# Performance work log

Hardware: AMD Instinct MI355X
Metric: run time of the kernel (lower is better)

The kernel has to match this reference:

```python
import jax, jax.numpy as jnp
import numpy as np

B, D, S = 16384, 2048, 512      # batch, input_dim, sideinfo_dim
E, H1, H2 = 8, 1024, 512        # subexpert_num, subexpert_unit
EPS = 1e-5                       # BatchNorm eps (torch default)


def setup_inputs() -> dict:
    key = jax.random.key(0)
    ks = jax.random.split(key, 16)
    inp = {
        "input": jax.random.normal(ks[0], (B, D), jnp.float32),
        "sideinfo": jax.random.normal(ks[1], (B, S), jnp.float32),
        # expert layer 1: Linear(D->H1) per expert, batched over E
        "W1": jax.random.normal(ks[2], (E, D, H1), jnp.float32) / np.sqrt(D),
        "b1": jax.random.normal(ks[3], (E, H1), jnp.float32) * 0.01,
        "gamma1": 1.0 + 0.01 * jax.random.normal(ks[4], (E, H1), jnp.float32),
        "beta1": jax.random.normal(ks[5], (E, H1), jnp.float32) * 0.01,
        "mean1": jax.random.normal(ks[6], (E, H1), jnp.float32) * 0.01,
        "var1": jax.random.uniform(ks[7], (E, H1), jnp.float32, 0.5, 1.5),
        # expert layer 2: Linear(H1->H2) per expert
        "W2": jax.random.normal(ks[8], (E, H1, H2), jnp.float32) / np.sqrt(H1),
        "b2": jax.random.normal(ks[9], (E, H2), jnp.float32) * 0.01,
        "gamma2": 1.0 + 0.01 * jax.random.normal(ks[10], (E, H2), jnp.float32),
        "beta2": jax.random.normal(ks[11], (E, H2), jnp.float32) * 0.01,
        "mean2": jax.random.normal(ks[12], (E, H2), jnp.float32) * 0.01,
        "var2": jax.random.uniform(ks[13], (E, H2), jnp.float32, 0.5, 1.5),
        # gate: Linear(S->E) + softmax
        "Wg": jax.random.normal(ks[14], (S, E), jnp.float32) / np.sqrt(S),
        "bg": jax.random.normal(ks[15], (E,), jnp.float32) * 0.01,
    }
    return inp


def _bn(x, gamma, beta, mean, var):
    # eval-mode BatchNorm1d with per-expert running stats; x: [B,E,H]
    return (x - mean) * (gamma * jax.lax.rsqrt(var + EPS)) + beta


def reference(input, sideinfo, W1, b1, gamma1, beta1, mean1, var1,
              W2, b2, gamma2, beta2, mean2, var2, Wg, bg):
    # all E expert MLPs as two batched GEMMs (dropout is identity in eval)
    h = jnp.einsum('bd,edh->beh', input, W1) + b1            # [B,E,H1]
    h = jax.nn.relu(_bn(h, gamma1, beta1, mean1, var1))
    o = jnp.einsum('beh,eho->beo', h, W2) + b2               # [B,E,H2]
    o = jax.nn.relu(_bn(o, gamma2, beta2, mean2, var2))
    gate = jax.nn.softmax(sideinfo @ Wg + bg, axis=1)        # [B,E]
    return jnp.einsum('beo,be->bo', o, gate)                 # [B,H2]
```

## Files before the change

kernel.cpp:

```cpp
#include <hip/hip_runtime.h>
#include <hip/hip_bf16.h>

static constexpr int B_  = 16384;
static constexpr int D_  = 2048;
static constexpr int S_  = 512;
static constexpr int E_  = 8;
static constexpr int H1_ = 1024;
static constexpr int H2_ = 512;
static constexpr float EPS_ = 1e-5f;

typedef __bf16 bf16x8 __attribute__((ext_vector_type(8)));
typedef float  f32x4  __attribute__((ext_vector_type(4)));

static __device__ __forceinline__ unsigned short f2bf(float f) {
    unsigned u = __float_as_uint(f);
    unsigned r = (u + 0x7fffu + ((u >> 16) & 1u)) >> 16;
    return (unsigned short)r;
}


__global__ void cvt_bf16_kernel(const float* __restrict__ in, ushort* __restrict__ out, long n) {
    long i = ((long)blockIdx.x * blockDim.x + threadIdx.x) * 4;
    long stride = (long)gridDim.x * blockDim.x * 4;
    for (; i < n; i += stride) {
        float4 v = *(const float4*)(in + i);
        ushort4 o;
        o.x = f2bf(v.x); o.y = f2bf(v.y); o.z = f2bf(v.z); o.w = f2bf(v.w);
        *(ushort4*)(out + i) = o;
    }
}

__global__ void transpose_cvt_kernel(const float* __restrict__ in, ushort* __restrict__ out,
                                     int R, int C) {
    __shared__ float t[64][65];
    int nbr = R >> 6, nbc = C >> 6;
    int bid = blockIdx.x;
    int e = bid / (nbr * nbc);
    int rem = bid % (nbr * nbc);
    int br = (rem / nbc) << 6, bc = (rem % nbc) << 6;
    const float* ip = in + (size_t)e * R * C;
    ushort* op = out + (size_t)e * R * C;
    int tcol = (threadIdx.x & 15) * 4;
    int trow = threadIdx.x >> 4;
#pragma unroll
    for (int p = 0; p < 4; p++) {
        int r = trow + p * 16;
        float4 v = *(const float4*)(ip + (size_t)(br + r) * C + bc + tcol);
        t[r][tcol + 0] = v.x; t[r][tcol + 1] = v.y; t[r][tcol + 2] = v.z; t[r][tcol + 3] = v.w;
    }
    __syncthreads();
#pragma unroll
    for (int p = 0; p < 4; p++) {
        int c = trow + p * 16;
        ushort4 o;
        o.x = f2bf(t[tcol + 0][c]);
        o.y = f2bf(t[tcol + 1][c]);
        o.z = f2bf(t[tcol + 2][c]);
        o.w = f2bf(t[tcol + 3][c]);
        *(ushort4*)(op + (size_t)(bc + c) * R + br + tcol) = o;
    }
}

__global__ void fold_bn_kernel(const float* __restrict__ gamma, const float* __restrict__ beta,
                               const float* __restrict__ mean, const float* __restrict__ var,
                               const float* __restrict__ bias,
                               float* __restrict__ Sv, float* __restrict__ Tv, int n) {
    int i = blockIdx.x * 256 + threadIdx.x;
    if (i < n) {
        float s = gamma[i] * rsqrtf(var[i] + EPS_);
        Sv[i] = s;
        Tv[i] = (bias[i] - mean[i]) * s + beta[i];
    }
}

__global__ void gate_kernel(const float* __restrict__ side, const float* __restrict__ Wg,
                            const float* __restrict__ bg, float* __restrict__ gate) {
    int wid = threadIdx.x >> 6, lane = threadIdx.x & 63;
    int b = blockIdx.x * 4 + wid;
    const float* sp = side + (size_t)b * S_ + lane * 8;
    float4 v0 = *(const float4*)sp;
    float4 v1 = *(const float4*)(sp + 4);
    float sv[8] = {v0.x, v0.y, v0.z, v0.w, v1.x, v1.y, v1.z, v1.w};
    float acc[E_] = {0,0,0,0,0,0,0,0};
    const float* wrow = Wg + (size_t)(lane * 8) * E_;
#pragma unroll
    for (int j = 0; j < 8; j++) {
        float4 w0 = *(const float4*)(wrow + j * E_);
        float4 w1 = *(const float4*)(wrow + j * E_ + 4);
        acc[0] += sv[j] * w0.x; acc[1] += sv[j] * w0.y;
        acc[2] += sv[j] * w0.z; acc[3] += sv[j] * w0.w;
        acc[4] += sv[j] * w1.x; acc[5] += sv[j] * w1.y;
        acc[6] += sv[j] * w1.z; acc[7] += sv[j] * w1.w;
    }
#pragma unroll
    for (int off = 32; off; off >>= 1)
#pragma unroll
        for (int e = 0; e < E_; e++) acc[e] += __shfl_xor(acc[e], off, 64);
    float m = -1e30f;
#pragma unroll
    for (int e = 0; e < E_; e++) { acc[e] += bg[e]; m = fmaxf(m, acc[e]); }
    float s = 0.f;
#pragma unroll
    for (int e = 0; e < E_; e++) { acc[e] = __expf(acc[e] - m); s += acc[e]; }
    float inv = 1.f / s;
    if (lane < E_) gate[(size_t)b * E_ + lane] = acc[lane] * inv;
}


__device__ __forceinline__ void g2lds16(const void* g, void* l) {
    __builtin_amdgcn_global_load_lds((const __attribute__((address_space(1))) unsigned int*)g,
                                     (__attribute__((address_space(3))) unsigned int*)l,
                                     16, 0, 0);
}

#define BAR()      asm volatile("s_barrier" ::: "memory")
#define WAITVM(n)  asm volatile("s_waitcnt vmcnt(" #n ")" ::: "memory")
#define MFMA(a,b,c) __builtin_amdgcn_mfma_f32_16x16x32_bf16((a),(b),(c),0,0,0)


template<int EPI>
__global__ __launch_bounds__(512, 2)
void gemm8(const ushort* __restrict__ A, const ushort* __restrict__ Bt, long aBatch,
           const float* __restrict__ Sv, const float* __restrict__ Tv,
           ushort* __restrict__ hout, float* __restrict__ outp, const float* __restrict__ gate,
           int M, int N, int K, int tilesN, int tilesM)
{
    extern __shared__ char smem[];

    const int NT  = K >> 6;
    const int tpe = tilesM * tilesN;

    const int nwg = gridDim.x, per = nwg >> 3;
    const int b0  = blockIdx.x;
    const int bid = (b0 & 7) * per + (b0 >> 3);

    const int e   = bid / tpe;
    const int rem = bid % tpe;
    const int tm  = rem / tilesN, tn = rem % tilesN;

    const char* aBase = (const char*)(A + (size_t)e * aBatch + (size_t)tm * 256 * K);
    const char* bBase = (const char*)(Bt + (size_t)e * N * K + (size_t)tn * 256 * K);
    const size_t rowB = (size_t)K * 2;
    const size_t half2 = 64 * rowB;
    const size_t half1 = 128 * rowB;

    const int tid = threadIdx.x, w = tid >> 6, lane = tid & 63;
    const int wm = w >> 2, wn = w & 3;

    const int srow = tid >> 3;
    const int scol_sw = ((tid & 7) * 16) ^ ((srow & 7) << 4);
    const int ldsW = w * 1024;

    const int lr = lane & 15;
    const int cks0 = ((lane >> 4) * 16) ^ ((lane & 7) << 4);
    const int cks1 = (64 + (lane >> 4) * 16) ^ ((lane & 7) << 4);
    const char* rdA0 = smem + 65536 + (wm * 128 + lr) * 128 + cks0;
    const char* rdA1 = smem + 65536 + (wm * 128 + lr) * 128 + cks1;
    const char* rdB0 = smem + (wn * 64 + lr) * 128 + cks0;
    const char* rdB1 = smem + (wn * 64 + lr) * 128 + cks1;

#define STG(gp, ldsoff) do { \
        g2lds16((gp), smem + (ldsoff)); \
        g2lds16((gp) + half2, smem + (ldsoff) + 8192); } while (0)

    const char* ga = aBase + (size_t)srow * rowB + scol_sw;
    const char* gb = bBase + (size_t)srow * rowB + scol_sw;

    f32x4 acc[8][4] = {};
    bf16x8 aC[4], aN[4], bC[4], bN[4];

    STG(ga,         65536 + 0 + 0     + ldsW);
    STG(ga + half1, 65536 + 0 + 16384 + ldsW);
    STG(gb,         0     + 0 + 0     + ldsW);
    STG(gb + half1, 0     + 0 + 16384 + ldsW);
    WAITVM(0);
    BAR();

#pragma unroll
    for (int mf = 0; mf < 4; ++mf) aC[mf] = *(const bf16x8*)(rdA0 + mf * 2048);
#pragma unroll
    for (int nf = 0; nf < 4; ++nf) bC[nf] = *(const bf16x8*)(rdB0 + nf * 2048);

    const char* spA0 = ga + 128;
    const char* spA1 = ga + half1 + 128;
    const char* spB0 = gb + 128;
    const char* spB1 = gb + half1 + 128;

#pragma unroll 2
    for (int t = 0; t < NT; ++t) {
        const int bi   = t & 1;
        const int oR   = bi * 32768;
        const int oRN  = (bi ^ 1) * 32768;
        const int oSA  = 65536 + (bi ^ 1) * 32768;
        const int oSB  = (bi ^ 1) * 32768;
        const bool more = (t < NT - 1);

#pragma unroll
        for (int mf = 0; mf < 4; ++mf) aN[mf] = *(const bf16x8*)(rdA0 + oR + (4 + mf) * 2048);
        if (more) {
            STG(spA0, oSA + 0 + ldsW);
            STG(spA1, oSA + 16384 + ldsW);
        }
        __builtin_amdgcn_s_setprio(1);
#pragma unroll
        for (int mf = 0; mf < 4; ++mf)
#pragma unroll
            for (int nf = 0; nf < 4; ++nf)
                acc[mf][nf] = MFMA(aC[mf], bC[nf], acc[mf][nf]);
        __builtin_amdgcn_s_setprio(0);

#pragma unroll
        for (int mf = 0; mf < 4; ++mf) aC[mf] = *(const bf16x8*)(rdA1 + oR + mf * 2048);
#pragma unroll
        for (int nf = 0; nf < 4; ++nf) bN[nf] = *(const bf16x8*)(rdB1 + oR + nf * 2048);
        if (more) STG(spB0, oSB + 0 + ldsW);
        __builtin_amdgcn_s_setprio(1);
#pragma unroll
        for (int mf = 0; mf < 4; ++mf)
#pragma unroll
            for (int nf = 0; nf < 4; ++nf)
                acc[4 + mf][nf] = MFMA(aN[mf], bC[nf], acc[4 + mf][nf]);
        __builtin_amdgcn_s_setprio(0);

#pragma unroll
        for (int mf = 0; mf < 4; ++mf) aN[mf] = *(const bf16x8*)(rdA1 + oR + (4 + mf) * 2048);
        if (more) STG(spB1, oSB + 16384 + ldsW);
        __builtin_amdgcn_s_setprio(1);
#pragma unroll
        for (int mf = 0; mf < 4; ++mf)
#pragma unroll
            for (int nf = 0; nf < 4; ++nf)
                acc[mf][nf] = MFMA(aC[mf], bN[nf], acc[mf][nf]);
        __builtin_amdgcn_s_setprio(0);

        __builtin_amdgcn_s_setprio(1);
#pragma unroll
        for (int mf = 0; mf < 4; ++mf)
#pragma unroll
            for (int nf = 0; nf < 4; ++nf)
                acc[4 + mf][nf] = MFMA(aN[mf], bN[nf], acc[4 + mf][nf]);
        __builtin_amdgcn_s_setprio(0);

        if (more) {
            WAITVM(0);
            BAR();
#pragma unroll
            for (int mf = 0; mf < 4; ++mf) aC[mf] = *(const bf16x8*)(rdA0 + oRN + mf * 2048);
#pragma unroll
            for (int nf = 0; nf < 4; ++nf) bC[nf] = *(const bf16x8*)(rdB0 + oRN + nf * 2048);
        }

        spA0 += 128; spA1 += 128; spB0 += 128; spB1 += 128;
    }

    const int rbase = tm * 256 + wm * 128 + (lane >> 4) * 4;
    const int cbase = tn * 256 + wn * 64 + lr;
    if (EPI == 1) {
#pragma unroll
        for (int nf = 0; nf < 4; ++nf) {
            const int col = cbase + nf * 16;
            const float s = Sv[e * N + col];
            const float tt = Tv[e * N + col];
#pragma unroll
            for (int mf = 0; mf < 8; ++mf) {
                const int row0 = rbase + mf * 16;
                f32x4 v = acc[mf][nf];
#pragma unroll
                for (int r = 0; r < 4; ++r) {
                    float x = v[r] * s + tt;
                    x = x > 0.f ? x : 0.f;
                    hout[((size_t)e * M + row0 + r) * N + col] = f2bf(x);
                }
            }
        }
    }
#undef STG
}


__global__ __launch_bounds__(512, 2)
void gemm2e(const ushort* __restrict__ H, const ushort* __restrict__ W2T,
            const float* __restrict__ Sv, const float* __restrict__ Tv,
            const float* __restrict__ gate, float* __restrict__ outp)
{
    extern __shared__ char smem[];

    const int b0 = blockIdx.x;
    const int bid = (b0 & 7) * 32 + (b0 >> 3);
    const int tm = bid >> 1, tn = bid & 1;

    const size_t rowB  = (size_t)H1_ * 2;
    const size_t strAE = (size_t)B_ * H1_ * 2;
    const size_t strBE = (size_t)H2_ * H1_ * 2;
    const size_t half2 = 64 * rowB;
    const size_t halfB = 128 * rowB;

    const int tid = threadIdx.x, w = tid >> 6, lane = tid & 63;
    const int wm = w >> 2, wn = w & 3;

    const int srow = tid >> 3;
    const int scol_sw = ((tid & 7) * 16) ^ ((srow & 7) << 4);
    const int ldsW = w * 1024;

    const int lr = lane & 15;
    const int cks0 = ((lane >> 4) * 16) ^ ((lane & 7) << 4);
    const int cks1 = (64 + (lane >> 4) * 16) ^ ((lane & 7) << 4);
    const char* rdA0 = smem + (wm * 64 + lr) * 128 + cks0;
    const char* rdA1 = smem + (wm * 64 + lr) * 128 + cks1;
    const char* rdB0 = smem + (wn * 64 + lr) * 128 + cks0;
    const char* rdB1 = smem + (wn * 64 + lr) * 128 + cks1;

    const char* ga = (const char*)H + (size_t)tm * 128 * rowB + (size_t)srow * rowB + scol_sw;
    const char* gb = (const char*)W2T + (size_t)tn * 256 * rowB + (size_t)srow * rowB + scol_sw;

#define STG6(gAp, gBp, aOff, bOff) do { \
        g2lds16((gAp),                 smem + (aOff) + 0     + ldsW); \
        g2lds16((gAp) + half2,         smem + (aOff) + 8192  + ldsW); \
        g2lds16((gBp),                 smem + (bOff) + 0     + ldsW); \
        g2lds16((gBp) + half2,         smem + (bOff) + 8192  + ldsW); \
        g2lds16((gBp) + halfB,         smem + (bOff) + 16384 + ldsW); \
        g2lds16((gBp) + halfB + half2, smem + (bOff) + 24576 + ldsW); } while (0)

    f32x4 acc[4][4] = {};
    f32x4 oacc[4][4] = {};
    bf16x8 a0[4], a1[4], b0v[4], b1v[4];

    int aCur = 98304, aN1 = 114688, aN2 = 131072;
    int bCur = 0,     bN1 = 32768,  bN2 = 65536;

    STG6(ga, gb, aCur, bCur);
    STG6(ga + 128, gb + 128, aN1, bN1);
    WAITVM(6);
    BAR();

#pragma unroll
    for (int mf = 0; mf < 4; ++mf) a0[mf] = *(const bf16x8*)(rdA0 + aCur + mf * 2048);
#pragma unroll
    for (int nf = 0; nf < 4; ++nf) b0v[nf] = *(const bf16x8*)(rdB0 + bCur + nf * 2048);

    const int rbase = tm * 128 + wm * 64 + (lane >> 4) * 4;
    const int cbase = tn * 256 + wn * 64 + lr;

    for (int t = 0; t < 128; ++t) {
        const int t2 = t + 2;
        const bool moreS = (t2 < 128);
        const bool moreT = (t < 127);

        const char* gA2 = ga + (size_t)(t2 >> 4) * strAE + (t2 & 15) * 128;
        const char* gB2 = gb + (size_t)(t2 >> 4) * strBE + (t2 & 15) * 128;

#pragma unroll
        for (int mf = 0; mf < 4; ++mf) a1[mf] = *(const bf16x8*)(rdA1 + aCur + mf * 2048);
#pragma unroll
        for (int nf = 0; nf < 4; ++nf) b1v[nf] = *(const bf16x8*)(rdB1 + bCur + nf * 2048);
        if (moreS) STG6(gA2, gB2, aN2, bN2);
        __builtin_amdgcn_s_setprio(1);
#pragma unroll
        for (int mf = 0; mf < 4; ++mf)
#pragma unroll
            for (int nf = 0; nf < 4; ++nf)
                acc[mf][nf] = MFMA(a0[mf], b0v[nf], acc[mf][nf]);
        __builtin_amdgcn_s_setprio(0);

        __builtin_amdgcn_s_setprio(1);
#pragma unroll
        for (int mf = 0; mf < 4; ++mf)
#pragma unroll
            for (int nf = 0; nf < 4; ++nf)
                acc[mf][nf] = MFMA(a1[mf], b1v[nf], acc[mf][nf]);
        __builtin_amdgcn_s_setprio(0);

        if (moreT) {
            if (moreS) { WAITVM(6); } else { WAITVM(0); }
            BAR();
#pragma unroll
            for (int mf = 0; mf < 4; ++mf) a0[mf] = *(const bf16x8*)(rdA0 + aN1 + mf * 2048);
#pragma unroll
            for (int nf = 0; nf < 4; ++nf) b0v[nf] = *(const bf16x8*)(rdB0 + bN1 + nf * 2048);
        }

        if ((t & 15) == 15) {
            const int e = t >> 4;
            float sc[4], tc[4];
#pragma unroll
            for (int nf = 0; nf < 4; ++nf) {
                sc[nf] = Sv[e * H2_ + cbase + nf * 16];
                tc[nf] = Tv[e * H2_ + cbase + nf * 16];
            }
#pragma unroll
            for (int mf = 0; mf < 4; ++mf) {
#pragma unroll
                for (int r = 0; r < 4; ++r) {
                    const int row = rbase + mf * 16 + r;
                    const float g = gate[(size_t)row * E_ + e];
#pragma unroll
                    for (int nf = 0; nf < 4; ++nf) {
                        float x = acc[mf][nf][r] * sc[nf] + tc[nf];
                        x = x > 0.f ? x : 0.f;
                        oacc[mf][nf][r] += g * x;
                    }
                }
            }
#pragma unroll
            for (int mf = 0; mf < 4; ++mf)
#pragma unroll
                for (int nf = 0; nf < 4; ++nf)
                    acc[mf][nf] = (f32x4){0.f, 0.f, 0.f, 0.f};
        }

        const int ta = aCur; aCur = aN1; aN1 = aN2; aN2 = ta;
        const int tb = bCur; bCur = bN1; bN1 = bN2; bN2 = tb;
    }

#pragma unroll
    for (int mf = 0; mf < 4; ++mf) {
#pragma unroll
        for (int r = 0; r < 4; ++r) {
            const int row = rbase + mf * 16 + r;
#pragma unroll
            for (int nf = 0; nf < 4; ++nf)
                outp[(size_t)row * H2_ + cbase + nf * 16] = oacc[mf][nf][r];
        }
    }
#undef STG6
}


extern "C" void kernel_launch(void* const* d_in, const int* in_sizes, int n_in,
                              void* d_out, int out_size, void* d_ws, size_t ws_size,
                              hipStream_t stream) {
    (void)in_sizes; (void)n_in; (void)out_size; (void)ws_size;

    const float* input    = (const float*)d_in[0];
    const float* sideinfo = (const float*)d_in[1];
    const float* W1   = (const float*)d_in[2];
    const float* b1   = (const float*)d_in[3];
    const float* g1   = (const float*)d_in[4];
    const float* be1  = (const float*)d_in[5];
    const float* m1   = (const float*)d_in[6];
    const float* v1   = (const float*)d_in[7];
    const float* W2   = (const float*)d_in[8];
    const float* b2   = (const float*)d_in[9];
    const float* g2   = (const float*)d_in[10];
    const float* be2  = (const float*)d_in[11];
    const float* m2   = (const float*)d_in[12];
    const float* v2   = (const float*)d_in[13];
    const float* Wg   = (const float*)d_in[14];
    const float* bg   = (const float*)d_in[15];

    char* w = (char*)d_ws;
    size_t off = 0;
    auto carve = [&](size_t bytes) {
        void* p = w + off;
        off += (bytes + 255) & ~(size_t)255;
        return p;
    };
    ushort* Abf  = (ushort*)carve((size_t)B_ * D_ * 2);
    ushort* W1T  = (ushort*)carve((size_t)E_ * H1_ * D_ * 2);
    ushort* W2T  = (ushort*)carve((size_t)E_ * H2_ * H1_ * 2);
    ushort* hbuf = (ushort*)carve((size_t)E_ * B_ * H1_ * 2);
    float*  S1   = (float*)carve((size_t)E_ * H1_ * 4);
    float*  T1   = (float*)carve((size_t)E_ * H1_ * 4);
    float*  S2   = (float*)carve((size_t)E_ * H2_ * 4);
    float*  T2   = (float*)carve((size_t)E_ * H2_ * 4);
    float*  gatep = (float*)carve((size_t)B_ * E_ * 4);

    float* outp = (float*)d_out;

    hipFuncSetAttribute(reinterpret_cast<const void*>(&gemm8<1>),
                        hipFuncAttributeMaxDynamicSharedMemorySize, 131072);
    hipFuncSetAttribute(reinterpret_cast<const void*>(&gemm2e),
                        hipFuncAttributeMaxDynamicSharedMemorySize, 147456);

    cvt_bf16_kernel<<<4096, 256, 0, stream>>>(input, Abf, (long)B_ * D_);
    transpose_cvt_kernel<<<E_ * (D_ / 64) * (H1_ / 64), 256, 0, stream>>>(W1, W1T, D_, H1_);
    transpose_cvt_kernel<<<E_ * (H1_ / 64) * (H2_ / 64), 256, 0, stream>>>(W2, W2T, H1_, H2_);
    fold_bn_kernel<<<(E_ * H1_ + 255) / 256, 256, 0, stream>>>(g1, be1, m1, v1, b1, S1, T1, E_ * H1_);
    fold_bn_kernel<<<(E_ * H2_ + 255) / 256, 256, 0, stream>>>(g2, be2, m2, v2, b2, S2, T2, E_ * H2_);
    gate_kernel<<<B_ / 4, 256, 0, stream>>>(sideinfo, Wg, bg, gatep);

    gemm8<1><<<E_ * (B_ / 256) * (H1_ / 256), 512, 131072, stream>>>(
        Abf, W1T, 0L, S1, T1, hbuf, nullptr, nullptr, B_, H1_, D_, H1_ / 256, B_ / 256);

    gemm2e<<<(B_ / 128) * (H2_ / 256), 512, 147456, stream>>>(
        hbuf, W2T, S2, T2, gatep, outp);
}
```

Before: 742.8 us.

## Triple-buffer B tiles in LDS to prefetch two K-steps ahead

Adds a third LDS buffer for the weight (B) operand in the first expert GEMM so its global-to-LDS copies are issued two iterations ahead, while A remains double-buffered. The wait before each barrier now allows the most recent B copy to stay in flight. This is meant to hide more global load latency behind MFMA work. In exchange, dynamic LDS grows to 160KB and buffer rotation logic adds register and control overhead.

Measured after the change: 705.2 us, median of 2. 1.05x faster.

```diff
diff --git a/kernel.cpp b/kernel.cpp
--- a/kernel.cpp
+++ b/kernel.cpp
@@ -154,8 +154,8 @@
     const int lr = lane & 15;
     const int cks0 = ((lane >> 4) * 16) ^ ((lane & 7) << 4);
     const int cks1 = (64 + (lane >> 4) * 16) ^ ((lane & 7) << 4);
-    const char* rdA0 = smem + 65536 + (wm * 128 + lr) * 128 + cks0;
-    const char* rdA1 = smem + 65536 + (wm * 128 + lr) * 128 + cks1;
+    const char* rdA0 = smem + 98304 + (wm * 128 + lr) * 128 + cks0;
+    const char* rdA1 = smem + 98304 + (wm * 128 + lr) * 128 + cks1;
     const char* rdB0 = smem + (wn * 64 + lr) * 128 + cks0;
     const char* rdB1 = smem + (wn * 64 + lr) * 128 + cks1;
 
@@ -169,11 +169,15 @@
     f32x4 acc[8][4] = {};
     bf16x8 aC[4], aN[4], bC[4], bN[4];
 
-    STG(ga,         65536 + 0 + 0     + ldsW);
-    STG(ga + half1, 65536 + 0 + 16384 + ldsW);
-    STG(gb,         0     + 0 + 0     + ldsW);
-    STG(gb + half1, 0     + 0 + 16384 + ldsW);
-    WAITVM(0);
+    int bCur = 0, bN1 = 32768, bN2 = 65536;
+
+    STG(ga,                98304 + 0 + 0     + ldsW);
+    STG(ga + half1,        98304 + 0 + 16384 + ldsW);
+    STG(gb,                0     + 0     + ldsW);
+    STG(gb + half1,        0     + 16384 + ldsW);
+    STG(gb + 128,          32768 + 0     + ldsW);
+    STG(gb + half1 + 128,  32768 + 16384 + ldsW);
+    WAITVM(4);
     BAR();
 
 #pragma unroll
@@ -183,21 +187,21 @@
 
     const char* spA0 = ga + 128;
     const char* spA1 = ga + half1 + 128;
-    const char* spB0 = gb + 128;
-    const char* spB1 = gb + half1 + 128;
+    const char* spB0 = gb + 256;
+    const char* spB1 = gb + half1 + 256;
 
 #pragma unroll 2
     for (int t = 0; t < NT; ++t) {
-        const int bi   = t & 1;
-        const int oR   = bi * 32768;
-        const int oRN  = (bi ^ 1) * 32768;
-        const int oSA  = 65536 + (bi ^ 1) * 32768;
-        const int oSB  = (bi ^ 1) * 32768;
-        const bool more = (t < NT - 1);
-
-#pragma unroll
-        for (int mf = 0; mf < 4; ++mf) aN[mf] = *(const bf16x8*)(rdA0 + oR + (4 + mf) * 2048);
-        if (more) {
+        const int bi    = t & 1;
+        const int oRA   = bi * 32768;
+        const int oRAN  = (bi ^ 1) * 32768;
+        const int oSA   = 98304 + (bi ^ 1) * 32768;
+        const bool moreA = (t < NT - 1);
+        const bool moreB = (t < NT - 2);
+
+#pragma unroll
+        for (int mf = 0; mf < 4; ++mf) aN[mf] = *(const bf16x8*)(rdA0 + oRA + (4 + mf) * 2048);
+        if (moreA) {
             STG(spA0, oSA + 0 + ldsW);
             STG(spA1, oSA + 16384 + ldsW);
         }
@@ -210,10 +214,10 @@
         __builtin_amdgcn_s_setprio(0);
 
 #pragma unroll
-        for (int mf = 0; mf < 4; ++mf) aC[mf] = *(const bf16x8*)(rdA1 + oR + mf * 2048);
-#pragma unroll
-        for (int nf = 0; nf < 4; ++nf) bN[nf] = *(const bf16x8*)(rdB1 + oR + nf * 2048);
-        if (more) STG(spB0, oSB + 0 + ldsW);
+        for (int mf = 0; mf < 4; ++mf) aC[mf] = *(const bf16x8*)(rdA1 + oRA + mf * 2048);
+#pragma unroll
+        for (int nf = 0; nf < 4; ++nf) bN[nf] = *(const bf16x8*)(rdB1 + bCur + nf * 2048);
+        if (moreB) STG(spB0, bN2 + 0 + ldsW);
         __builtin_amdgcn_s_setprio(1);
 #pragma unroll
         for (int mf = 0; mf < 4; ++mf)
@@ -223,8 +227,8 @@
         __builtin_amdgcn_s_setprio(0);
 
 #pragma unroll
-        for (int mf = 0; mf < 4; ++mf) aN[mf] = *(const bf16x8*)(rdA1 + oR + (4 + mf) * 2048);
-        if (more) STG(spB1, oSB + 16384 + ldsW);
+        for (int mf = 0; mf < 4; ++mf) aN[mf] = *(const bf16x8*)(rdA1 + oRA + (4 + mf) * 2048);
+        if (moreB) STG(spB1, bN2 + 16384 + ldsW);
         __builtin_amdgcn_s_setprio(1);
 #pragma unroll
         for (int mf = 0; mf < 4; ++mf)
@@ -241,16 +245,17 @@
                 acc[4 + mf][nf] = MFMA(aN[mf], bN[nf], acc[4 + mf][nf]);
         __builtin_amdgcn_s_setprio(0);
 
-        if (more) {
-            WAITVM(0);
+        if (moreA) {
+            if (moreB) { WAITVM(4); } else { WAITVM(0); }
             BAR();
 #pragma unroll
-            for (int mf = 0; mf < 4; ++mf) aC[mf] = *(const bf16x8*)(rdA0 + oRN + mf * 2048);
-#pragma unroll
-            for (int nf = 0; nf < 4; ++nf) bC[nf] = *(const bf16x8*)(rdB0 + oRN + nf * 2048);
+            for (int mf = 0; mf < 4; ++mf) aC[mf] = *(const bf16x8*)(rdA0 + oRAN + mf * 2048);
+#pragma unroll
+            for (int nf = 0; nf < 4; ++nf) bC[nf] = *(const bf16x8*)(rdB0 + bN1 + nf * 2048);
         }
 
         spA0 += 128; spA1 += 128; spB0 += 128; spB1 += 128;
+        const int tb = bCur; bCur = bN1; bN1 = bN2; bN2 = tb;
     }
 
     const int rbase = tm * 256 + wm * 128 + (lane >> 4) * 4;
@@ -468,7 +473,7 @@
     float* outp = (float*)d_out;
 
     hipFuncSetAttribute(reinterpret_cast<const void*>(&gemm8<1>),
-                        hipFuncAttributeMaxDynamicSharedMemorySize, 131072);
+                        hipFuncAttributeMaxDynamicSharedMemorySize, 163840);
     hipFuncSetAttribute(reinterpret_cast<const void*>(&gemm2e),
                         hipFuncAttributeMaxDynamicSharedMemorySize, 147456);
 
@@ -479,7 +484,7 @@
     fold_bn_kernel<<<(E_ * H2_ + 255) / 256, 256, 0, stream>>>(g2, be2, m2, v2, b2, S2, T2, E_ * H2_);
     gate_kernel<<<B_ / 4, 256, 0, stream>>>(sideinfo, Wg, bg, gatep);
 
-    gemm8<1><<<E_ * (B_ / 256) * (H1_ / 256), 512, 131072, stream>>>(
+    gemm8<1><<<E_ * (B_ / 256) * (H1_ / 256), 512, 163840, stream>>>(
         Abf, W1T, 0L, S1, T1, hbuf, nullptr, nullptr, B_, H1_, D_, H1_ / 256, B_ / 256);
 
     gemm2e<<<(B_ / 128) * (H2_ / 256), 512, 147456, stream>>>(
```
